# Performance work log

Hardware: AMD Instinct MI355X
Metric: run time of the kernel (lower is better)

## Reference

```python
import jax, jax.numpy as jnp
import numpy as np

LN_EPS = 1e-5
NEG_SLOPE = 0.01  # torch LeakyReLU default


def layernorm(x, w, b):
    m = jnp.mean(x, axis=-1, keepdims=True)
    v = jnp.mean((x - m) ** 2, axis=-1, keepdims=True)
    return (x - m) * jax.lax.rsqrt(v + LN_EPS) * w + b


def setup_inputs() -> dict:
    key = jax.random.key(0)
    ks = jax.random.split(key, 12)
    B, T, C, E = 16, 1024, 768, 2
    d = C
    s = 0.02
    inp = {
        "x": jax.random.normal(ks[0], (B, T, C), jnp.float32),
        "ln1_w": jnp.ones((C,), jnp.float32),
        "ln1_b": jnp.zeros((C,), jnp.float32),
        "wqkv": jax.random.normal(ks[1], (C, 3 * C), jnp.float32) * s,
        "bqkv": jnp.zeros((3 * C,), jnp.float32),
        "wproj": jax.random.normal(ks[2], (C, C), jnp.float32) * s,
        "bproj": jnp.zeros((C,), jnp.float32),
        "ln2_w": jnp.ones((C,), jnp.float32),
        "ln2_b": jnp.zeros((C,), jnp.float32),
        "wg": jax.random.normal(ks[3], (C, E), jnp.float32) * s,
        # Experts module uses torch.randn (std 1); we scale down for numerics
        "w1": jax.random.normal(ks[4], (E, d, 4 * d), jnp.float32) * s,
        "w2": jax.random.normal(ks[5], (E, 4 * d, 4 * d), jnp.float32) * s,
        "w3": jax.random.normal(ks[6], (E, 4 * d, d), jnp.float32) * s,
        "n_head": 12,
    }
    return inp


def block_forward(x, ln1_w, ln1_b, wqkv, bqkv, wproj, bproj,
                  ln2_w, ln2_b, wg, w1, w2, w3, n_head):
    B, T, C = x.shape
    H = n_head
    hd = C // H
    E = wg.shape[-1]

    # ---- causal self-attention + residual ----
    h = layernorm(x, ln1_w, ln1_b)
    qkv = h @ wqkv + bqkv                      # [B,T,3C]
    q, k, v = jnp.split(qkv, 3, axis=-1)
    q = q.reshape(B, T, H, hd).transpose(0, 2, 1, 3)  # bhtd
    k = k.reshape(B, T, H, hd).transpose(0, 2, 1, 3)
    v = v.reshape(B, T, H, hd).transpose(0, 2, 1, 3)
    scores = jnp.einsum('bhqd,bhkd->bhqk', q, k) / jnp.sqrt(jnp.float32(hd))
    causal = jnp.tril(jnp.ones((T, T), bool))
    scores = jnp.where(causal, scores, jnp.finfo(scores.dtype).min)
    attn = jax.nn.softmax(scores, axis=-1)
    y = jnp.einsum('bhqk,bhkd->bhqd', attn, v)
    y = y.transpose(0, 2, 1, 3).reshape(B, T, C)
    x = x + (y @ wproj + bproj)

    # ---- MoE (top-2 gating, capacity dispatch) + residual ----
    h2 = layernorm(x, ln2_w, ln2_b)
    capacity = (T * 2) // E                    # capacity_factor = 1.0, top-2
    raw_gates = jax.nn.softmax(h2 @ wg, axis=-1)   # [B,T,E]

    idx1 = jnp.argmax(raw_gates, axis=-1)
    mask1 = jax.nn.one_hot(idx1, E, dtype=raw_gates.dtype)
    gate1 = jnp.sum(raw_gates * mask1, axis=-1)    # [B,T]
    gates2 = raw_gates * (1.0 - mask1)
    idx2 = jnp.argmax(gates2, axis=-1)
    mask2 = jax.nn.one_hot(idx2, E, dtype=raw_gates.dtype)
    gate2 = jnp.sum(raw_gates * mask2, axis=-1)
    denom = gate1 + gate2 + 1e-9
    gate1, gate2 = gate1 / denom, gate2 / denom

    # aux load-balancing loss (before capacity truncation)
    density = jnp.mean(mask1, axis=1)              # [B,E]
    density_proxy = jnp.mean(raw_gates, axis=1)    # [B,E]
    aux_loss = jnp.mean(density * density_proxy) * (E * E)

    # positions within each expert buffer (exclusive cumsum over tokens)
    pos1 = jnp.cumsum(mask1, axis=1) - mask1       # [B,T,E]
    mask1 = mask1 * (pos1 < capacity)
    mask1_count = jnp.sum(mask1, axis=1, keepdims=True)
    pos2 = (jnp.cumsum(mask2, axis=1) - mask2) + mask1_count
    mask2 = mask2 * (pos2 < capacity)

    oh1 = jax.nn.one_hot(pos1.astype(jnp.int32), capacity, dtype=raw_gates.dtype)
    oh2 = jax.nn.one_hot(pos2.astype(jnp.int32), capacity, dtype=raw_gates.dtype)
    combine = (gate1[..., None] * mask1)[..., None] * oh1 \
            + (gate2[..., None] * mask2)[..., None] * oh2   # [B,T,E,C]
    dispatch = (combine > 0).astype(h2.dtype)

    # dispatch -> per-expert batches
    expert_in = jnp.einsum('bnd,bnec->ebcd', h2, dispatch)   # [E,B,Cap,d]
    Bc = B * capacity
    ei = expert_in.reshape(E, Bc, C)
    lrelu = lambda z: jnp.where(z >= 0, z, NEG_SLOPE * z)
    hh = lrelu(jnp.einsum('end,edh->enh', ei, w1))
    hh = lrelu(jnp.einsum('end,edh->enh', hh, w2))
    eo = jnp.einsum('end,edh->enh', hh, w3).reshape(E, B, capacity, C)
    moe_out = jnp.einsum('ebcd,bnec->bnd', eo, combine)

    x = x + moe_out
    return x, aux_loss


def reference(x, ln1_w, ln1_b, wqkv, bqkv, wproj, bproj,
              ln2_w, ln2_b, wg, w1, w2, w3, n_head):
    return block_forward(x, ln1_w, ln1_b, wqkv, bqkv, wproj, bproj,
                         ln2_w, ln2_b, wg, w1, w2, w3, n_head)
```

## Files before the change

kernel.cpp:

```cpp
#include <hip/hip_runtime.h>
#include <cstdint>
#include <cstddef>

constexpr int B_  = 16;
constexpr int T_  = 1024;
constexpr int C_  = 768;
constexpr int H_  = 12;
constexpr int HD_ = 64;
constexpr int BT_ = B_ * T_;
constexpr int C3_ = 3 * C_;
constexpr int QK2_ = 2 * C_;
constexpr int FF_ = 4 * C_;
constexpr int MCH_ = 8192;

typedef __bf16 bf16x8 __attribute__((ext_vector_type(8)));
typedef float  floatx4 __attribute__((ext_vector_type(4)));
typedef unsigned short u16x8 __attribute__((ext_vector_type(8)));

__device__ inline float bf2f(unsigned short u) {
  union { unsigned int i; float f; } x; x.i = ((unsigned int)u) << 16; return x.f;
}
__device__ inline unsigned short f2bf(float f) {
  union { float f; unsigned int i; } x; x.f = f;
  unsigned int u = x.i;
  u += 0x7fffu + ((u >> 16) & 1u);
  return (unsigned short)(u >> 16);
}

#define GLOAD_LDS16(gp, lp)                                              \
  __builtin_amdgcn_global_load_lds(                                      \
      (__attribute__((address_space(1))) void*)(gp),                     \
      (__attribute__((address_space(3))) void*)(lp), 16, 0, 0)

template <bool GATE>
__launch_bounds__(256)
__global__ void ln_kernel(const float* __restrict__ x, const float* __restrict__ w,
                          const float* __restrict__ b, unsigned short* __restrict__ out,
                          const float* __restrict__ wg, float* __restrict__ gates) {
  int row = blockIdx.x;
  int tid = threadIdx.x;
  const float* xr = x + (size_t)row * C_;
  float v0 = xr[tid], v1 = xr[tid + 256], v2 = xr[tid + 512];
  float s  = v0 + v1 + v2;
  float ss = v0 * v0 + v1 * v1 + v2 * v2;
#pragma unroll
  for (int off = 32; off > 0; off >>= 1) {
    s  += __shfl_down(s, off, 64);
    ss += __shfl_down(ss, off, 64);
  }
  __shared__ float red[8];
  int wid = tid >> 6;
  if ((tid & 63) == 0) { red[wid] = s; red[4 + wid] = ss; }
  __syncthreads();
  float st  = red[0] + red[1] + red[2] + red[3];
  float sst = red[4] + red[5] + red[6] + red[7];
  float mean = st * (1.0f / C_);
  float var  = sst * (1.0f / C_) - mean * mean;
  float rstd = rsqrtf(var + 1e-5f);
  float h0 = (v0 - mean) * rstd * w[tid]       + b[tid];
  float h1 = (v1 - mean) * rstd * w[tid + 256] + b[tid + 256];
  float h2 = (v2 - mean) * rstd * w[tid + 512] + b[tid + 512];
  unsigned short* orow = out + (size_t)row * C_;
  orow[tid]       = f2bf(h0);
  orow[tid + 256] = f2bf(h1);
  orow[tid + 512] = f2bf(h2);

  if (GATE) {
    float a0 = h0 * wg[2 * tid]     + h1 * wg[2 * (tid + 256)]     + h2 * wg[2 * (tid + 512)];
    float a1 = h0 * wg[2 * tid + 1] + h1 * wg[2 * (tid + 256) + 1] + h2 * wg[2 * (tid + 512) + 1];
#pragma unroll
    for (int off = 32; off > 0; off >>= 1) {
      a0 += __shfl_down(a0, off, 64);
      a1 += __shfl_down(a1, off, 64);
    }
    __shared__ float redg[8];
    if ((tid & 63) == 0) { redg[wid] = a0; redg[4 + wid] = a1; }
    __syncthreads();
    if (tid == 0) {
      float A0 = redg[0] + redg[1] + redg[2] + redg[3];
      float A1 = redg[4] + redg[5] + redg[6] + redg[7];
      float m  = fmaxf(A0, A1);
      float e0 = __expf(A0 - m), e1 = __expf(A1 - m);
      float invs = 1.0f / (e0 + e1);
      const float gnorm = 1.0f / (1.0f + 1e-9f);
      gates[2 * row]     = e0 * invs * gnorm;
      gates[2 * row + 1] = e1 * invs * gnorm;
    }
  }
}

struct CtJobs {
  const float* in[8];
  unsigned short* out[8];
  int K[8], N[8], tX[8];
  int t0[9];
};

__launch_bounds__(256)
__global__ void convT_batch(CtJobs J) {
  __shared__ float t[32][33];
  int bid = blockIdx.x;
  int ji = 0;
#pragma unroll
  for (int i = 0; i < 7; ++i) ji += (bid >= J.t0[i + 1]) ? 1 : 0;
  const float* in = J.in[ji];
  unsigned short* out = J.out[ji];
  const int K = J.K[ji], N = J.N[ji];
  const int lt = bid - J.t0[ji];
  const int bx = lt % J.tX[ji], by = lt / J.tX[ji];
  const int n0 = bx * 32, k0 = by * 32;
  const int tx = threadIdx.x & 31, ty = threadIdx.x >> 5;
#pragma unroll
  for (int r = 0; r < 32; r += 8)
    t[r + ty][tx] = in[(size_t)(k0 + r + ty) * N + n0 + tx];
  __syncthreads();
#pragma unroll
  for (int r = 0; r < 32; r += 8)
    out[(size_t)(n0 + r + ty) * K + k0 + tx] = f2bf(t[tx][r + ty]);
}

template <int ACT, bool BIAS, bool RES, bool COMBINE, bool OUTBF16,
          bool VSPLIT = false, bool ZB = false>
__launch_bounds__(256)
__global__ void gemm_bf16(const unsigned short* __restrict__ A,
                          const unsigned short* __restrict__ Bt,
                          const float* __restrict__ bias,
                          const float* __restrict__ Rres,
                          const float* __restrict__ gates2, int eidx,
                          void* __restrict__ Cout,
                          unsigned short* __restrict__ vtout,
                          int M, int N, int K,
                          size_t zsA, size_t zsB) {
  __shared__ __attribute__((aligned(16))) unsigned short Als[8192];
  __shared__ __attribute__((aligned(16))) unsigned short Bls[8192];
  const int tid  = threadIdx.x;
  const int wave = tid >> 6, lane = tid & 63;
  const int wr = wave >> 1, wc = wave & 1;

  if (ZB) {
    A  += (size_t)blockIdx.z * zsA;
    Bt += (size_t)blockIdx.z * zsB;
    eidx = (int)blockIdx.z;
  }

  int bx = blockIdx.x, by = blockIdx.y;
  {
    const int nbx = gridDim.x;
    const int nwg = nbx * gridDim.y;
    if ((nwg & 7) == 0) {
      const int bid = by * nbx + bx;
      const int swz = (bid & 7) * (nwg >> 3) + (bid >> 3);
      by = swz / nbx; bx = swz - by * nbx;
    }
  }
  const int m0 = by * 128, n0 = bx * 128;

  const int srow = wave * 32 + (lane >> 3);
  const int skg  = (lane & 7) ^ ((lane >> 3) & 7);
  const unsigned short* Ap = A  + (size_t)(m0 + srow) * K + skg * 8;
  const unsigned short* Bp = Bt + (size_t)(n0 + srow) * K + skg * 8;
  unsigned short* AlsW = Als + wave * 2048;
  unsigned short* BlsW = Bls + wave * 2048;

  floatx4 acc[4][4];
#pragma unroll
  for (int i = 0; i < 4; ++i)
#pragma unroll
    for (int j = 0; j < 4; ++j) acc[i][j] = floatx4{0.f, 0.f, 0.f, 0.f};

  const int q  = lane >> 4;
  const int ml = lane & 15;
  const int rsw = ml & 7;

  for (int k0 = 0; k0 < K; k0 += 64) {
    __syncthreads();
#pragma unroll
    for (int i = 0; i < 4; ++i) {
      GLOAD_LDS16(Ap + (size_t)(i * 8) * K + k0, AlsW + i * 512);
      GLOAD_LDS16(Bp + (size_t)(i * 8) * K + k0, BlsW + i * 512);
    }
    __syncthreads();
#pragma unroll
    for (int ks = 0; ks < 2; ++ks) {
      const int p = (ks * 4 + q) ^ rsw;
      bf16x8 af[4], bfg[4];
#pragma unroll
      for (int i = 0; i < 4; ++i) {
        int ar = wr * 64 + i * 16 + ml;
        af[i]  = *(const bf16x8*)&Als[(ar * 8 + p) * 8];
        int br = wc * 64 + i * 16 + ml;
        bfg[i] = *(const bf16x8*)&Bls[(br * 8 + p) * 8];
      }
#pragma unroll
      for (int i = 0; i < 4; ++i)
#pragma unroll
        for (int j = 0; j < 4; ++j)
          acc[i][j] = __builtin_amdgcn_mfma_f32_16x16x32_bf16(af[i], bfg[j], acc[i][j], 0, 0, 0);
    }
  }

  const int rbase = q * 4;
#pragma unroll
  for (int i = 0; i < 4; ++i) {
    int row = m0 + wr * 64 + i * 16 + rbase;
#pragma unroll
    for (int j = 0; j < 4; ++j) {
      int col = n0 + wc * 64 + j * 16 + ml;
      float bcol = BIAS ? bias[col] : 0.f;
#pragma unroll
      for (int r = 0; r < 4; ++r) {
        float v = acc[i][j][r];
        if (BIAS) v += bcol;
        if (ACT == 1) v = (v >= 0.f) ? v : 0.01f * v;
        if (RES) v += Rres[(size_t)(row + r) * N + col];
        if (COMBINE) {
          float g = gates2[2 * (row + r) + eidx];
          float* op = (float*)Cout + (size_t)(row + r) * N + col;
          if (ZB) atomicAdd(op, g * v);
          else    *op += g * v;
        } else if (VSPLIT) {
          if (col < QK2_) {
            ((unsigned short*)Cout)[(size_t)(row + r) * QK2_ + col] = f2bf(v);
          } else {
            vtout[(size_t)(col - QK2_) * BT_ + row + r] = f2bf(v);
          }
        } else if (OUTBF16) {
          ((unsigned short*)Cout)[(size_t)(row + r) * N + col] = f2bf(v);
        } else {
          ((float*)Cout)[(size_t)(row + r) * N + col] = v;
        }
      }
    }
  }
}

#define GB256_BAR()   asm volatile("s_barrier" ::: "memory")
#define GB256_LGKM0() asm volatile("s_waitcnt lgkmcnt(0)" ::: "memory")

template <int ACT, bool BIAS>
__launch_bounds__(512, 2)
__global__ void gemm256(const unsigned short* __restrict__ A,
                        const unsigned short* __restrict__ Bt,
                        const float* __restrict__ bias,
                        unsigned short* __restrict__ Cout,
                        int M, int N, int K,
                        size_t zsA, size_t zsB, size_t zsC) {
  __shared__ __attribute__((aligned(16))) unsigned short L[65536];
  const int tid = threadIdx.x;
  const int w = tid >> 6, l = tid & 63;
  const int wr = w >> 2, wc = w & 3;
  const int ml = l & 15, q = l >> 4;

  A    += (size_t)blockIdx.z * zsA;
  Bt   += (size_t)blockIdx.z * zsB;
  Cout += (size_t)blockIdx.z * zsC;

  int bx = blockIdx.x, by = blockIdx.y;
  {
    const int nbx = gridDim.x;
    const int nwg = nbx * gridDim.y;
    if ((nwg & 7) == 0) {
      const int bid = by * nbx + bx;
      const int swz = (bid & 7) * (nwg >> 3) + (bid >> 3);
      by = swz / nbx; bx = swz - by * nbx;
    }
  }
  const int m0 = by * 256, n0 = bx * 256;

  const int srow = l >> 2;
  const int sg   = ((l & 3) ^ ((l >> 3) & 3)) * 8;
  const unsigned short* Ast = A  + (size_t)(m0 + srow) * K + sg;
  const unsigned short* Bst = Bt + (size_t)(n0 + srow) * K + sg;
  const int ldsw = w * 1024;

#define STG(cb, mat, ks, srcp, kk)                                           \
  do {                                                                       \
    const unsigned short* _s = (srcp) + (size_t)(w * 32) * K + (kk) + (ks) * 32; \
    unsigned short* _d = L + (cb) * 32768 + (mat) * 16384 + (ks) * 8192 + ldsw;  \
    GLOAD_LDS16(_s, _d);                                                     \
    GLOAD_LDS16(_s + (size_t)16 * K, _d + 512);                              \
  } while (0)

  const int dphys = (q ^ ((ml >> 1) & 3)) * 8;
  const int aoff = (wr * 128 + ml) * 32 + dphys;
  const int boff = (wc * 64 + ml) * 32 + dphys;

  floatx4 acc[8][4];
#pragma unroll
  for (int m = 0; m < 8; ++m)
#pragma unroll
    for (int n = 0; n < 4; ++n) acc[m][n] = floatx4{0.f, 0.f, 0.f, 0.f};

  const int NT = K >> 6;

  STG(0, 0, 0, Ast, 0);  STG(0, 1, 0, Bst, 0);
  STG(0, 0, 1, Ast, 0);  STG(0, 1, 1, Bst, 0);
  STG(1, 0, 0, Ast, 64); STG(1, 1, 0, Bst, 64);
  asm volatile("s_waitcnt vmcnt(0)" ::: "memory");
  GB256_BAR();

  for (int j = 0; j < NT; ++j) {
    const int c = j & 1, nx = c ^ 1;
    const int kk1 = (j + 1) << 6, kk2 = (j + 2) << 6;
    const bool st1 = (j + 1 < NT), st2 = (j + 2 < NT);
    bf16x8 bA[4], bB[4];

#define LOAD_A(KS, MH)                                                       \
  _Pragma("unroll")                                                          \
  for (int mq = 0; mq < 4; ++mq)                                             \
    bA[mq] = *(const bf16x8*)&L[c * 32768 + (KS) * 8192 + aoff + ((MH) * 4 + mq) * 512];
#define LOAD_B(KS)                                                           \
  _Pragma("unroll")                                                          \
  for (int n = 0; n < 4; ++n)                                                \
    bB[n] = *(const bf16x8*)&L[c * 32768 + 16384 + (KS) * 8192 + boff + n * 512];
#define MFMA16(MH)                                                           \
  __builtin_amdgcn_s_setprio(1);                                             \
  _Pragma("unroll")                                                          \
  for (int mq = 0; mq < 4; ++mq)                                             \
    _Pragma("unroll")                                                        \
    for (int n = 0; n < 4; ++n)                                              \
      acc[(MH) * 4 + mq][n] = __builtin_amdgcn_mfma_f32_16x16x32_bf16(       \
          bA[mq], bB[n], acc[(MH) * 4 + mq][n], 0, 0, 0);                    \
  __builtin_amdgcn_s_setprio(0);

    LOAD_B(0); LOAD_A(0, 0);
    if (st1) STG(nx, 0, 1, Ast, kk1);
    GB256_BAR(); GB256_LGKM0();
    MFMA16(0);
    GB256_BAR();

    LOAD_A(0, 1);
    if (st1) STG(nx, 1, 1, Bst, kk1);
    GB256_BAR(); GB256_LGKM0();
    MFMA16(1);
    GB256_BAR();

    LOAD_B(1); LOAD_A(1, 0);
    if (st2) STG(c, 0, 0, Ast, kk2);
    GB256_BAR(); GB256_LGKM0();
    MFMA16(0);
    GB256_BAR();

    LOAD_A(1, 1);
    if (st2) STG(c, 1, 0, Bst, kk2);
    GB256_BAR(); GB256_LGKM0();
    MFMA16(1);
    if (st2)      asm volatile("s_waitcnt vmcnt(4)" ::: "memory");
    else if (st1) asm volatile("s_waitcnt vmcnt(0)" ::: "memory");
    GB256_BAR();
#undef LOAD_A
#undef LOAD_B
#undef MFMA16
  }

#pragma unroll
  for (int m = 0; m < 8; ++m) {
    const int row = m0 + wr * 128 + m * 16 + q * 4;
#pragma unroll
    for (int n = 0; n < 4; ++n) {
      const int col = n0 + wc * 64 + n * 16 + ml;
      const float bcol = BIAS ? bias[col] : 0.f;
#pragma unroll
      for (int r = 0; r < 4; ++r) {
        float v = acc[m][n][r];
        if (BIAS) v += bcol;
        if (ACT == 1) v = (v >= 0.f) ? v : 0.01f * v;
        Cout[(size_t)(row + r) * N + col] = f2bf(v);
      }
    }
  }
#undef STG
}

__launch_bounds__(512)
__global__ void attn_kernel(const unsigned short* __restrict__ qk,
                            const unsigned short* __restrict__ vT,
                            unsigned short* __restrict__ y) {
  __shared__ __attribute__((aligned(16))) unsigned short Qls[128 * 64];
  __shared__ __attribute__((aligned(16))) unsigned short K2[2][64 * 64];
  __shared__ __attribute__((aligned(16))) unsigned short V2[2][64 * 64];
  __shared__ __attribute__((aligned(16))) unsigned short Pls[8 * 16 * 72];

  const int tid  = threadIdx.x;
  const int wave = tid >> 6, lane = tid & 63;
  const int quad = lane >> 4, n = lane & 15;
  const int q0 = blockIdx.x * 128;
  const int bh = blockIdx.y;
  const int b = bh / H_, h = bh % H_;
  const size_t qbase = (size_t)b * T_ * QK2_ + (size_t)h * HD_;
  const size_t vbase = (size_t)h * HD_ * BT_ + (size_t)b * T_;

  const int r8 = lane >> 3;
  const int g  = (lane & 7) ^ r8;

#pragma unroll
  for (int i = 0; i < 2; ++i) {
    int row = wave * 16 + i * 8 + r8;
    GLOAD_LDS16(qk + qbase + (size_t)(q0 + row) * QK2_ + g * 8,
                Qls + wave * 1024 + i * 512);
  }

#define STAGE_KV(bf, k0)                                                      \
  do {                                                                        \
    int row = wave * 8 + r8;                                                  \
    GLOAD_LDS16(qk + qbase + (size_t)((k0) + row) * QK2_ + C_ + g * 8,        \
                K2[bf] + wave * 512);                                         \
    GLOAD_LDS16(vT + vbase + (size_t)row * BT_ + (k0) + g * 8,                \
                V2[bf] + wave * 512);                                         \
  } while (0)

  STAGE_KV(0, 0);

  floatx4 O[4];
#pragma unroll
  for (int ct = 0; ct < 4; ++ct) O[ct] = floatx4{0.f, 0.f, 0.f, 0.f};
  float mrow[4] = {-1e30f, -1e30f, -1e30f, -1e30f};
  float lrow[4] = {0.f, 0.f, 0.f, 0.f};

  const int nkt = 2 * blockIdx.x + 2;
  const int dt  = 2 * blockIdx.x + (wave >> 2);
  unsigned short* Pw = Pls + wave * (16 * 72);

  for (int kt = 0; kt < nkt; ++kt) {
    const int cur = kt & 1;
    __syncthreads();
    if (kt + 1 < nkt) STAGE_KV(cur ^ 1, (kt + 1) << 6);
    if (kt > dt) continue;

    floatx4 sacc[4];
#pragma unroll
    for (int ct = 0; ct < 4; ++ct) sacc[ct] = floatx4{0.f, 0.f, 0.f, 0.f};
#pragma unroll
    for (int ks = 0; ks < 2; ++ks) {
      const int ga = (ks * 4 + quad) ^ (n & 7);
      bf16x8 aq = *(const bf16x8*)&Qls[((wave * 16 + n) * 8 + ga) * 8];
#pragma unroll
      for (int ct = 0; ct < 4; ++ct) {
        bf16x8 kb = *(const bf16x8*)&K2[cur][((ct * 16 + n) * 8 + ga) * 8];
        sacc[ct] = __builtin_amdgcn_mfma_f32_16x16x32_bf16(aq, kb, sacc[ct], 0, 0, 0);
      }
    }

    float p[4][4];
#pragma unroll
    for (int ct = 0; ct < 4; ++ct)
#pragma unroll
      for (int r = 0; r < 4; ++r) p[ct][r] = sacc[ct][r] * 0.125f;
    if (kt == dt) {
      const int kgb = (kt << 6) + n, qgb = q0 + wave * 16 + quad * 4;
#pragma unroll
      for (int ct = 0; ct < 4; ++ct)
#pragma unroll
        for (int r = 0; r < 4; ++r)
          if (kgb + ct * 16 > qgb + r) p[ct][r] = -1e30f;
    }
#pragma unroll
    for (int r = 0; r < 4; ++r) {
      float tm = fmaxf(fmaxf(p[0][r], p[1][r]), fmaxf(p[2][r], p[3][r]));
      tm = fmaxf(tm, __shfl_xor(tm, 1, 64));
      tm = fmaxf(tm, __shfl_xor(tm, 2, 64));
      tm = fmaxf(tm, __shfl_xor(tm, 4, 64));
      tm = fmaxf(tm, __shfl_xor(tm, 8, 64));
      float mn = fmaxf(mrow[r], tm);
      float alpha = __expf(mrow[r] - mn);
      mrow[r] = mn;
      float ps = 0.f;
#pragma unroll
      for (int ct = 0; ct < 4; ++ct) {
        float pe = __expf(p[ct][r] - mn);
        p[ct][r] = pe;
        ps += pe;
      }
      ps += __shfl_xor(ps, 1, 64);
      ps += __shfl_xor(ps, 2, 64);
      ps += __shfl_xor(ps, 4, 64);
      ps += __shfl_xor(ps, 8, 64);
      lrow[r] = lrow[r] * alpha + ps;
      O[0][r] *= alpha; O[1][r] *= alpha; O[2][r] *= alpha; O[3][r] *= alpha;
    }

#pragma unroll
    for (int ct = 0; ct < 4; ++ct)
#pragma unroll
      for (int r = 0; r < 4; ++r)
        Pw[(quad * 4 + r) * 72 + ct * 16 + n] = f2bf(p[ct][r]);

#pragma unroll
    for (int ks = 0; ks < 2; ++ks) {
      bf16x8 pa = *(const bf16x8*)&Pw[n * 72 + (ks * 4 + quad) * 8];
      const int gv = (ks * 4 + quad) ^ (n & 7);
#pragma unroll
      for (int ct = 0; ct < 4; ++ct) {
        bf16x8 vb = *(const bf16x8*)&V2[cur][((ct * 16 + n) * 8 + gv) * 8];
        O[ct] = __builtin_amdgcn_mfma_f32_16x16x32_bf16(pa, vb, O[ct], 0, 0, 0);
      }
    }
  }

#pragma unroll
  for (int r = 0; r < 4; ++r) {
    float inv = 1.0f / lrow[r];
    int row = q0 + wave * 16 + quad * 4 + r;
    unsigned short* dst = y + ((size_t)b * T_ + row) * C_ + h * HD_;
#pragma unroll
    for (int ct = 0; ct < 4; ++ct)
      dst[ct * 16 + n] = f2bf(O[ct][r] * inv);
  }
#undef STAGE_KV
}

__launch_bounds__(1024)
__global__ void moe_stats_kernel(const float* __restrict__ gates,
                                 float* __restrict__ out_aux) {
  int wave = threadIdx.x >> 6, lane = threadIdx.x & 63;
  float c0 = 0.f, sp0 = 0.f, sp1 = 0.f;
#pragma unroll
  for (int j = 0; j < 16; ++j) {
    int t = wave * T_ + lane + 64 * j;
    float p0 = gates[2 * t], p1 = gates[2 * t + 1];
    c0  += (p1 > p0) ? 0.f : 1.f;
    sp0 += p0;
    sp1 += p1;
  }
#pragma unroll
  for (int off = 32; off > 0; off >>= 1) {
    c0  += __shfl_down(c0, off, 64);
    sp0 += __shfl_down(sp0, off, 64);
    sp1 += __shfl_down(sp1, off, 64);
  }
  __shared__ float red[16][3];
  if (lane == 0) { red[wave][0] = c0; red[wave][1] = sp0; red[wave][2] = sp1; }
  __syncthreads();
  if (threadIdx.x == 0) {
    float s = 0.f;
    for (int b = 0; b < B_; ++b) {
      float cc0 = red[b][0];
      float d0 = cc0 * (1.f / T_), d1 = (T_ - cc0) * (1.f / T_);
      float px0 = red[b][1] * (1.f / T_), px1 = red[b][2] * (1.f / T_);
      s += d0 * px0 + d1 * px1;
    }
    out_aux[0] = s * (4.f / 32.f);
  }
}

extern "C" void kernel_launch(void* const* d_in, const int* in_sizes, int n_in,
                              void* d_out, int out_size, void* d_ws, size_t ws_size,
                              hipStream_t stream) {
  const float* x     = (const float*)d_in[0];
  const float* ln1_w = (const float*)d_in[1];
  const float* ln1_b = (const float*)d_in[2];
  const float* wqkv  = (const float*)d_in[3];
  const float* bqkv  = (const float*)d_in[4];
  const float* wproj = (const float*)d_in[5];
  const float* bproj = (const float*)d_in[6];
  const float* ln2_w = (const float*)d_in[7];
  const float* ln2_b = (const float*)d_in[8];
  const float* wg    = (const float*)d_in[9];
  const float* w1    = (const float*)d_in[10];
  const float* w2    = (const float*)d_in[11];
  const float* w3    = (const float*)d_in[12];
  float* out = (float*)d_out;

  unsigned short* wsu   = (unsigned short*)d_ws;
  unsigned short* wqkvT = wsu;
  unsigned short* wprojT= wqkvT + (size_t)C3_ * C_;
  unsigned short* w1T   = wprojT + (size_t)C_ * C_;
  unsigned short* w2T   = w1T + (size_t)2 * FF_ * C_;
  unsigned short* w3T   = w2T + (size_t)2 * FF_ * FF_;
  unsigned short* hb    = w3T + (size_t)2 * C_ * FF_;
  unsigned short* region= hb + (size_t)BT_ * C_;
  unsigned short* qkb   = region;
  unsigned short* vTb   = region + (size_t)BT_ * QK2_;
  unsigned short* yb    = region + (size_t)BT_ * 3 * C_;

  const size_t regionElems = (size_t)BT_ * 4 * C_;
  const size_t bigElems    = (size_t)4 * MCH_ * FF_;
  const size_t baseElems   = (size_t)(region - wsu);
  const bool   big = ws_size >= (baseElems + bigElems + 65536) * sizeof(unsigned short);

  float* gates = (float*)(region + (big ? bigElems : regionElems));

  {
    CtJobs J;
    int idx = 0, acc = 0;
    auto add = [&](const float* in, unsigned short* outp, int K, int N) {
      J.in[idx] = in; J.out[idx] = outp; J.K[idx] = K; J.N[idx] = N;
      J.tX[idx] = N / 32; J.t0[idx] = acc;
      acc += (N / 32) * (K / 32);
      ++idx;
    };
    add(wqkv, wqkvT, C_, C3_);
    add(wproj, wprojT, C_, C_);
    for (int e = 0; e < 2; ++e) {
      add(w1 + (size_t)e * C_ * FF_, w1T + (size_t)e * FF_ * C_, C_, FF_);
      add(w2 + (size_t)e * FF_ * FF_, w2T + (size_t)e * FF_ * FF_, FF_, FF_);
      add(w3 + (size_t)e * FF_ * C_, w3T + (size_t)e * C_ * FF_, FF_, C_);
    }
    J.t0[8] = acc;
    convT_batch<<<acc, 256, 0, stream>>>(J);
  }

  ln_kernel<false><<<BT_, 256, 0, stream>>>(x, ln1_w, ln1_b, hb, nullptr, nullptr);
  gemm_bf16<0, true, false, false, true, true><<<dim3(C3_ / 128, BT_ / 128), 256, 0, stream>>>(
      hb, wqkvT, bqkv, nullptr, nullptr, 0, qkb, vTb, BT_, C3_, C_, 0, 0);
  attn_kernel<<<dim3(T_ / 128, B_ * H_), 512, 0, stream>>>(qkb, vTb, yb);
  gemm_bf16<0, true, true, false, false><<<dim3(C_ / 128, BT_ / 128), 256, 0, stream>>>(
      yb, wprojT, bproj, x, nullptr, 0, out, nullptr, BT_, C_, C_, 0, 0);

  ln_kernel<true><<<BT_, 256, 0, stream>>>(out, ln2_w, ln2_b, hb, wg, gates);
  moe_stats_kernel<<<1, 1024, 0, stream>>>(gates, out + (size_t)BT_ * C_);

  if (big) {
    unsigned short* hh1b = region;
    unsigned short* hh2b = region + (size_t)2 * MCH_ * FF_;
    for (int c = 0; c < BT_ / MCH_; ++c) {
      const unsigned short* a = hb + (size_t)c * MCH_ * C_;
      gemm256<1, false><<<dim3(FF_ / 256, MCH_ / 256, 2), 512, 0, stream>>>(
          a, w1T, nullptr, hh1b, MCH_, FF_, C_,
          0, (size_t)FF_ * C_, (size_t)MCH_ * FF_);
      gemm256<1, false><<<dim3(FF_ / 256, MCH_ / 256, 2), 512, 0, stream>>>(
          hh1b, w2T, nullptr, hh2b, MCH_, FF_, FF_,
          (size_t)MCH_ * FF_, (size_t)FF_ * FF_, (size_t)MCH_ * FF_);
      gemm_bf16<0, false, false, true, false, false, true>
          <<<dim3(C_ / 128, MCH_ / 128, 2), 256, 0, stream>>>(
          hh2b, w3T, nullptr, nullptr,
          gates + (size_t)2 * c * MCH_, 0, out + (size_t)c * MCH_ * C_, nullptr,
          MCH_, C_, FF_, (size_t)MCH_ * FF_, (size_t)C_ * FF_);
    }
  } else {
    unsigned short* hh1 = region;
    unsigned short* hh2 = region + (size_t)MCH_ * FF_;
    for (int e = 0; e < 2; ++e) {
      for (int c = 0; c < BT_ / MCH_; ++c) {
        const unsigned short* a = hb + (size_t)c * MCH_ * C_;
        gemm_bf16<1, false, false, false, true><<<dim3(FF_ / 128, MCH_ / 128), 256, 0, stream>>>(
            a, w1T + (size_t)e * FF_ * C_, nullptr, nullptr, nullptr, 0, hh1, nullptr,
            MCH_, FF_, C_, 0, 0);
        gemm_bf16<1, false, false, false, true><<<dim3(FF_ / 128, MCH_ / 128), 256, 0, stream>>>(
            hh1, w2T + (size_t)e * FF_ * FF_, nullptr, nullptr, nullptr, 0, hh2, nullptr,
            MCH_, FF_, FF_, 0, 0);
        gemm_bf16<0, false, false, true, false><<<dim3(C_ / 128, MCH_ / 128), 256, 0, stream>>>(
            hh2, w3T + (size_t)e * C_ * FF_, nullptr, nullptr,
            gates + (size_t)2 * c * MCH_, e, out + (size_t)c * MCH_ * C_, nullptr,
            MCH_, C_, FF_, 0, 0);
      }
    }
  }
}
```

Measured before the change: 1.593 ms.

## Replace z-batched expert GEMMs with full-batch per-expert launches; add MFMA priority in attention

The big-workspace MoE path stops batching both experts through blockIdx.z over token chunks. It now loops over experts and runs each GEMM over all tokens, which removes the atomicAdd in the combine epilogue in favour of a plain read-modify-write. The attention kernel also raises wave priority around its MFMA blocks with s_setprio. The trade-off is a different workspace requirement and launch structure: six large launches replace z-batched ones, which may change occupancy and L2 reuse of weights.

```diff
diff --git a/kernel.cpp b/kernel.cpp
--- a/kernel.cpp
+++ b/kernel.cpp
@@ -120,7 +120,7 @@
 }
 
 template <int ACT, bool BIAS, bool RES, bool COMBINE, bool OUTBF16,
-          bool VSPLIT = false, bool ZB = false>
+          bool VSPLIT = false>
 __launch_bounds__(256)
 __global__ void gemm_bf16(const unsigned short* __restrict__ A,
                           const unsigned short* __restrict__ Bt,
@@ -129,19 +129,12 @@
                           const float* __restrict__ gates2, int eidx,
                           void* __restrict__ Cout,
                           unsigned short* __restrict__ vtout,
-                          int M, int N, int K,
-                          size_t zsA, size_t zsB) {
+                          int M, int N, int K) {
   __shared__ __attribute__((aligned(16))) unsigned short Als[8192];
   __shared__ __attribute__((aligned(16))) unsigned short Bls[8192];
   const int tid  = threadIdx.x;
   const int wave = tid >> 6, lane = tid & 63;
   const int wr = wave >> 1, wc = wave & 1;
-
-  if (ZB) {
-    A  += (size_t)blockIdx.z * zsA;
-    Bt += (size_t)blockIdx.z * zsB;
-    eidx = (int)blockIdx.z;
-  }
 
   int bx = blockIdx.x, by = blockIdx.y;
   {
@@ -216,8 +209,7 @@
         if (COMBINE) {
           float g = gates2[2 * (row + r) + eidx];
           float* op = (float*)Cout + (size_t)(row + r) * N + col;
-          if (ZB) atomicAdd(op, g * v);
-          else    *op += g * v;
+          *op += g * v;
         } else if (VSPLIT) {
           if (col < QK2_) {
             ((unsigned short*)Cout)[(size_t)(row + r) * QK2_ + col] = f2bf(v);
@@ -243,17 +235,12 @@
                         const unsigned short* __restrict__ Bt,
                         const float* __restrict__ bias,
                         unsigned short* __restrict__ Cout,
-                        int M, int N, int K,
-                        size_t zsA, size_t zsB, size_t zsC) {
+                        int M, int N, int K) {
   __shared__ __attribute__((aligned(16))) unsigned short L[65536];
   const int tid = threadIdx.x;
   const int w = tid >> 6, l = tid & 63;
   const int wr = w >> 2, wc = w & 3;
   const int ml = l & 15, q = l >> 4;
-
-  A    += (size_t)blockIdx.z * zsA;
-  Bt   += (size_t)blockIdx.z * zsB;
-  Cout += (size_t)blockIdx.z * zsC;
 
   int bx = blockIdx.x, by = blockIdx.y;
   {
@@ -430,6 +417,7 @@
     floatx4 sacc[4];
 #pragma unroll
     for (int ct = 0; ct < 4; ++ct) sacc[ct] = floatx4{0.f, 0.f, 0.f, 0.f};
+    __builtin_amdgcn_s_setprio(1);
 #pragma unroll
     for (int ks = 0; ks < 2; ++ks) {
       const int ga = (ks * 4 + quad) ^ (n & 7);
@@ -440,6 +428,7 @@
         sacc[ct] = __builtin_amdgcn_mfma_f32_16x16x32_bf16(aq, kb, sacc[ct], 0, 0, 0);
       }
     }
+    __builtin_amdgcn_s_setprio(0);
 
     float p[4][4];
 #pragma unroll
@@ -485,6 +474,7 @@
       for (int r = 0; r < 4; ++r)
         Pw[(quad * 4 + r) * 72 + ct * 16 + n] = f2bf(p[ct][r]);
 
+    __builtin_amdgcn_s_setprio(1);
 #pragma unroll
     for (int ks = 0; ks < 2; ++ks) {
       bf16x8 pa = *(const bf16x8*)&Pw[n * 72 + (ks * 4 + quad) * 8];
@@ -495,6 +485,7 @@
         O[ct] = __builtin_amdgcn_mfma_f32_16x16x32_bf16(pa, vb, O[ct], 0, 0, 0);
       }
     }
+    __builtin_amdgcn_s_setprio(0);
   }
 
 #pragma unroll
@@ -574,9 +565,9 @@
   unsigned short* yb    = region + (size_t)BT_ * 3 * C_;
 
   const size_t regionElems = (size_t)BT_ * 4 * C_;
-  const size_t bigElems    = (size_t)4 * MCH_ * FF_;
+  const size_t bigElems    = (size_t)2 * BT_ * FF_;
   const size_t baseElems   = (size_t)(region - wsu);
-  const bool   big = ws_size >= (baseElems + bigElems + 65536) * sizeof(unsigned short);
+  const bool   big  = ws_size >= (baseElems + bigElems + 65536) * sizeof(unsigned short);
 
   float* gates = (float*)(region + (big ? bigElems : regionElems));
 
@@ -602,30 +593,25 @@
 
   ln_kernel<false><<<BT_, 256, 0, stream>>>(x, ln1_w, ln1_b, hb, nullptr, nullptr);
   gemm_bf16<0, true, false, false, true, true><<<dim3(C3_ / 128, BT_ / 128), 256, 0, stream>>>(
-      hb, wqkvT, bqkv, nullptr, nullptr, 0, qkb, vTb, BT_, C3_, C_, 0, 0);
+      hb, wqkvT, bqkv, nullptr, nullptr, 0, qkb, vTb, BT_, C3_, C_);
   attn_kernel<<<dim3(T_ / 128, B_ * H_), 512, 0, stream>>>(qkb, vTb, yb);
   gemm_bf16<0, true, true, false, false><<<dim3(C_ / 128, BT_ / 128), 256, 0, stream>>>(
-      yb, wprojT, bproj, x, nullptr, 0, out, nullptr, BT_, C_, C_, 0, 0);
+      yb, wprojT, bproj, x, nullptr, 0, out, nullptr, BT_, C_, C_);
 
   ln_kernel<true><<<BT_, 256, 0, stream>>>(out, ln2_w, ln2_b, hb, wg, gates);
   moe_stats_kernel<<<1, 1024, 0, stream>>>(gates, out + (size_t)BT_ * C_);
 
   if (big) {
     unsigned short* hh1b = region;
-    unsigned short* hh2b = region + (size_t)2 * MCH_ * FF_;
-    for (int c = 0; c < BT_ / MCH_; ++c) {
-      const unsigned short* a = hb + (size_t)c * MCH_ * C_;
-      gemm256<1, false><<<dim3(FF_ / 256, MCH_ / 256, 2), 512, 0, stream>>>(
-          a, w1T, nullptr, hh1b, MCH_, FF_, C_,
-          0, (size_t)FF_ * C_, (size_t)MCH_ * FF_);
-      gemm256<1, false><<<dim3(FF_ / 256, MCH_ / 256, 2), 512, 0, stream>>>(
-          hh1b, w2T, nullptr, hh2b, MCH_, FF_, FF_,
-          (size_t)MCH_ * FF_, (size_t)FF_ * FF_, (size_t)MCH_ * FF_);
-      gemm_bf16<0, false, false, true, false, false, true>
-          <<<dim3(C_ / 128, MCH_ / 128, 2), 256, 0, stream>>>(
-          hh2b, w3T, nullptr, nullptr,
-          gates + (size_t)2 * c * MCH_, 0, out + (size_t)c * MCH_ * C_, nullptr,
-          MCH_, C_, FF_, (size_t)MCH_ * FF_, (size_t)C_ * FF_);
+    unsigned short* hh2b = region + (size_t)BT_ * FF_;
+    for (int e = 0; e < 2; ++e) {
+      gemm256<1, false><<<dim3(FF_ / 256, BT_ / 256), 512, 0, stream>>>(
+          hb, w1T + (size_t)e * FF_ * C_, nullptr, hh1b, BT_, FF_, C_);
+      gemm256<1, false><<<dim3(FF_ / 256, BT_ / 256), 512, 0, stream>>>(
+          hh1b, w2T + (size_t)e * FF_ * FF_, nullptr, hh2b, BT_, FF_, FF_);
+      gemm_bf16<0, false, false, true, false><<<dim3(C_ / 128, BT_ / 128), 256, 0, stream>>>(
+          hh2b, w3T + (size_t)e * C_ * FF_, nullptr, nullptr,
+          gates, e, out, nullptr, BT_, C_, FF_);
     }
   } else {
     unsigned short* hh1 = region;
@@ -635,14 +621,14 @@
         const unsigned short* a = hb + (size_t)c * MCH_ * C_;
         gemm_bf16<1, false, false, false, true><<<dim3(FF_ / 128, MCH_ / 128), 256, 0, stream>>>(
             a, w1T + (size_t)e * FF_ * C_, nullptr, nullptr, nullptr, 0, hh1, nullptr,
-            MCH_, FF_, C_, 0, 0);
+            MCH_, FF_, C_);
         gemm_bf16<1, false, false, false, true><<<dim3(FF_ / 128, MCH_ / 128), 256, 0, stream>>>(
             hh1, w2T + (size_t)e * FF_ * FF_, nullptr, nullptr, nullptr, 0, hh2, nullptr,
-            MCH_, FF_, FF_, 0, 0);
+            MCH_, FF_, FF_);
         gemm_bf16<0, false, false, true, false><<<dim3(C_ / 128, MCH_ / 128), 256, 0, stream>>>(
             hh2, w3T + (size_t)e * C_ * FF_, nullptr, nullptr,
             gates + (size_t)2 * c * MCH_, e, out + (size_t)c * MCH_ * C_, nullptr,
-            MCH_, C_, FF_, 0, 0);
+            MCH_, C_, FF_);
       }
     }
   }
```

Result: faster. 1.505 ms (-5.5%).
